# Performance work log

Hardware: AMD Instinct MI355X
Metric: run time of the kernel (lower is better)

The kernel has to match this reference:

```python
import jax, jax.numpy as jnp
import numpy as np

B, L, S, D, H = 2, 384, 384, 512, 256
BASE_TEMP = 10.0
LN_EPS = 1e-5


def setup_inputs() -> dict:
    key = jax.random.key(0)
    ks = jax.random.split(key, 12)
    return {
        "q": jax.random.normal(ks[0], (B, L, D), jnp.float32),
        "k": jax.random.normal(ks[1], (B, S, D), jnp.float32),
        "q_global": jax.random.normal(ks[2], (B, D), jnp.float32),
        "k_global": jax.random.normal(ks[3], (B, D), jnp.float32),
        "W1": jax.random.normal(ks[4], (4 * D, H), jnp.float32) * (1.0 / np.sqrt(4 * D)),
        "b1": jnp.zeros((H,), jnp.float32),
        "gamma": jnp.ones((H,), jnp.float32),
        "beta": jnp.zeros((H,), jnp.float32),
        "W2": jax.random.normal(ks[5], (H, 1), jnp.float32) * (1.0 / np.sqrt(H)),
        "b2": jnp.zeros((1,), jnp.float32),
        "gumbel_u": jax.random.uniform(ks[6], (B, L, S, 2), jnp.float32),
    }


def reference(q, k, q_global, k_global, W1, b1, gamma, beta, W2, b2, gumbel_u):
    d = q.shape[-1]
    # Decompose Linear(4D,H) on the [q, k, q_global, k_global] concat into
    # four per-tensor projections; sum broadcasts to the pairwise grid.
    Wq, Wk, Wqg, Wkg = jnp.split(W1, 4, axis=0)  # each [D,H]
    hq = q @ Wq + (q_global @ Wqg)[:, None, :]   # [B,L,H]
    hk = k @ Wk + (k_global @ Wkg)[:, None, :]   # [B,S,H]
    h = hq[:, :, None, :] + hk[:, None, :, :] + b1  # [B,L,S,H]
    h = jax.nn.gelu(h, approximate=False)
    mu = jnp.mean(h, axis=-1, keepdims=True)
    var = jnp.mean(jnp.square(h - mu), axis=-1, keepdims=True)
    h = (h - mu) * jax.lax.rsqrt(var + LN_EPS) * gamma + beta
    thresholds = (h @ W2)[..., 0] + b2[0]  # [B,L,S]
    sim = jnp.einsum("bld,bsd->bls", q, k) / jnp.sqrt(jnp.float32(d))
    logits = (sim - thresholds) / BASE_TEMP
    binary_logits = jnp.stack([-logits, logits], axis=-1)  # [B,L,S,2]
    u = jnp.clip(gumbel_u, 1e-6, 1.0 - 1e-6)
    g = -jnp.log(-jnp.log(u))
    soft = jax.nn.softmax(binary_logits + g, axis=-1)  # tau=1.0
    hard = jax.nn.one_hot(jnp.argmax(soft, axis=-1), 2, dtype=soft.dtype)
    y = hard + soft - jax.lax.stop_gradient(soft)  # straight-through
    return y[..., 1][:, None, :, :]  # [B,1,L,S]
```

## Files before the change

kernel.cpp:

```cpp
#include <hip/hip_runtime.h>
#include <hip/hip_bf16.h>
#include <math.h>

#define Bb 2
#define Lq 384
#define Sk 384
#define Dd 512
#define Hh 256

#define LIST_CAP 65536
#define NROWS (2 * Bb * Lq)

#define HQD_OFF  0
#define HKD_OFF  (HQD_OFF + Bb*Lq*Hh*8)
#define PART_OFF (HKD_OFF + Bb*Sk*Hh*8)
#define GQD_OFF  (PART_OFF + NROWS*4*Hh*8)
#define GKD_OFF  (GQD_OFF + Bb*Hh*8)
#define HQ_OFF   (GKD_OFF + Bb*Hh*8)
#define HK_OFF   (HQ_OFF + Bb*Lq*Hh*4)
#define SIM0_OFF (HK_OFF + Bb*Sk*Hh*4)
#define SIM1_OFF (SIM0_OFF + Bb*Lq*Sk*4)
#define SCAL_OFF (SIM1_OFF + Bb*Lq*Sk*4)
#define CNT_OFF  (SCAL_OFF + 64)
#define LIST_OFF (CNT_OFF + 64)

__global__ __launch_bounds__(256) void proj_fused_kernel(
    const float* __restrict__ q, const float* __restrict__ k,
    const float* __restrict__ qg, const float* __restrict__ kg,
    const float* __restrict__ W1,
    const float* __restrict__ gam, const float* __restrict__ bet,
    const float* __restrict__ W2, const float* __restrict__ b2,
    double* __restrict__ gq_d, double* __restrict__ gk_d,
    float* __restrict__ scal, int* __restrict__ cnt,
    double* __restrict__ part)
{
    __shared__ double red[64][5];
    __shared__ float2 red2[256];
    __shared__ __align__(16) float tile[4][128];
    int bx  = blockIdx.x;
    int tid = threadIdx.x;
    if (bx < 16) {
        int isK = bx & 1;
        int b   = (bx >> 1) & 1;
        int hc  = bx >> 2;
        int hl  = tid >> 2;
        int dp  = tid & 3;
        int h   = hc * 64 + hl;
        const float* gv = (isK ? kg : qg) + b * Dd;
        const float* wp = W1 + (isK ? 3 : 2) * Dd * Hh + h;
        int d0 = dp * 128;
        double a0 = 0, a1 = 0, a2 = 0, a3 = 0;
        for (int i = 0; i < 128; i += 4) {
            int d = d0 + i;
            a0 = fma((double)gv[d + 0], (double)wp[(d + 0) * Hh], a0);
            a1 = fma((double)gv[d + 1], (double)wp[(d + 1) * Hh], a1);
            a2 = fma((double)gv[d + 2], (double)wp[(d + 2) * Hh], a2);
            a3 = fma((double)gv[d + 3], (double)wp[(d + 3) * Hh], a3);
        }
        red[hl][dp] = ((a0 + a1) + (a2 + a3));
        __syncthreads();
        if (dp == 0) {
            double s = (red[hl][0] + red[hl][1]) + (red[hl][2] + red[hl][3]);
            (isK ? gk_d : gq_d)[b * Hh + h] = s;
        }
    } else if (bx == 16) {
        if (tid == 0) *cnt = 0;
        float w2v = W2[tid];
        red2[tid] = make_float2(gam[tid] * w2v, bet[tid] * w2v);
        __syncthreads();
        for (int o = 128; o > 0; o >>= 1) {
            if (tid < o) {
                red2[tid].x += red2[tid + o].x;
                red2[tid].y += red2[tid + o].y;
            }
            __syncthreads();
        }
        if (tid == 0) {
            scal[0] = red2[0].x;
            scal[1] = red2[0].y + b2[0];
        }
    } else {
        int bxp = bx - 17;
        int ds  = bxp & 3;
        int rgid = bxp >> 2;
        bool isQ = rgid < 192;
        int bb = isQ ? rgid : rgid - 192;
        int b  = bb / 96;
        int rg = bb % 96;
        const float* src = isQ ? q : k;
        int woff = isQ ? 0 : Dd * Hh;
        int rowbase = b * Lq + rg * 4;

        if (tid < 128) {
            int row = tid >> 5;
            int c4  = (tid & 31) << 2;
            *reinterpret_cast<float4*>(&tile[row][c4]) =
                *reinterpret_cast<const float4*>(
                    src + (size_t)(rowbase + row) * Dd + ds * 128 + c4);
        }
        __syncthreads();

        const float* wp = W1 + woff + (ds * 128) * Hh + tid;
        double a0 = 0.0, a1 = 0.0, a2 = 0.0, a3 = 0.0;
#pragma unroll 2
        for (int d4 = 0; d4 < 128; d4 += 4) {
            double w0 = (double)wp[(d4 + 0) * Hh];
            double w1 = (double)wp[(d4 + 1) * Hh];
            double w2 = (double)wp[(d4 + 2) * Hh];
            double w3 = (double)wp[(d4 + 3) * Hh];
            float4 t0 = *reinterpret_cast<const float4*>(&tile[0][d4]);
            float4 t1 = *reinterpret_cast<const float4*>(&tile[1][d4]);
            float4 t2 = *reinterpret_cast<const float4*>(&tile[2][d4]);
            float4 t3 = *reinterpret_cast<const float4*>(&tile[3][d4]);
            a0 = fma((double)t0.x, w0, a0); a0 = fma((double)t0.y, w1, a0);
            a0 = fma((double)t0.z, w2, a0); a0 = fma((double)t0.w, w3, a0);
            a1 = fma((double)t1.x, w0, a1); a1 = fma((double)t1.y, w1, a1);
            a1 = fma((double)t1.z, w2, a1); a1 = fma((double)t1.w, w3, a1);
            a2 = fma((double)t2.x, w0, a2); a2 = fma((double)t2.y, w1, a2);
            a2 = fma((double)t2.z, w2, a2); a2 = fma((double)t2.w, w3, a2);
            a3 = fma((double)t3.x, w0, a3); a3 = fma((double)t3.y, w1, a3);
            a3 = fma((double)t3.z, w2, a3); a3 = fma((double)t3.w, w3, a3);
        }
        int rowglob = (isQ ? 0 : Bb * Lq) + rowbase;
        size_t obase = ((size_t)rowglob * 4 + ds) * Hh + tid;
        part[obase]           = a0;
        part[obase + 4 * Hh]  = a1;
        part[obase + 8 * Hh]  = a2;
        part[obase + 12 * Hh] = a3;
    }
}

__global__ __launch_bounds__(256) void finalize_kernel(
    const double* __restrict__ part,
    const double* __restrict__ gq_d, const double* __restrict__ gk_d,
    const float* __restrict__ b1,
    double* __restrict__ hq_d, double* __restrict__ hk_d,
    float* __restrict__ hq, float* __restrict__ hk)
{
    int tid = threadIdx.x;
    int bx  = blockIdx.x;
#pragma unroll
    for (int r = 0; r < 2; ++r) {
        int rowglob = bx * 2 + r;
        bool isQ = rowglob < Bb * Lq;
        int rr = isQ ? rowglob : rowglob - Bb * Lq;
        int b  = rr / Lq;
        size_t pbase = ((size_t)rowglob * 4) * Hh + tid;
        double p0 = part[pbase];
        double p1 = part[pbase + 1 * Hh];
        double p2 = part[pbase + 2 * Hh];
        double p3 = part[pbase + 3 * Hh];
        double gl = (isQ ? gq_d : gk_d)[b * Hh + tid];
        double tot = ((p0 + p1) + (p2 + p3)) + gl;
        size_t o = (size_t)rr * Hh + tid;
        if (isQ) {
            hq_d[o] = tot;
            hq[o]   = (float)(tot + (double)b1[tid]);
        } else {
            hk_d[o] = tot;
            hk[o]   = (float)tot;
        }
    }
}

__global__ __launch_bounds__(256) void sim_kernel(
    const float* __restrict__ q, const float* __restrict__ k,
    float* __restrict__ sim01)
{
    __shared__ __align__(16) float qs[32][132];
    __shared__ __align__(16) float ks[32][132];
    int tid = threadIdx.x;
    int bx = blockIdx.x;
    int kc = (bx >= Bb * 144) ? 1 : 0;
    int r  = bx - kc * Bb * 144;
    int b  = r / 144;  r %= 144;
    int lt = r / 12, st = r % 12;
    int tl = tid >> 4, ts = tid & 15;
    const float* qb = q + (b * Lq + lt * 32) * Dd;
    const float* kb = k + (b * Sk + st * 32) * Dd;
    float a00 = 0.f, a01 = 0.f, a10 = 0.f, a11 = 0.f;
    for (int c = kc * 256; c < kc * 256 + 256; c += 128) {
        __syncthreads();
        for (int i = tid; i < 1024; i += 256) {
            int row = i >> 5;
            int c4  = (i & 31) << 2;
            *reinterpret_cast<float4*>(&qs[row][c4]) =
                *reinterpret_cast<const float4*>(qb + row * Dd + c + c4);
            *reinterpret_cast<float4*>(&ks[row][c4]) =
                *reinterpret_cast<const float4*>(kb + row * Dd + c + c4);
        }
        __syncthreads();
#pragma unroll 2
        for (int dd = 0; dd < 128; dd += 4) {
            float4 q0 = *reinterpret_cast<const float4*>(&qs[tl][dd]);
            float4 q1 = *reinterpret_cast<const float4*>(&qs[tl + 16][dd]);
            float4 k0 = *reinterpret_cast<const float4*>(&ks[ts][dd]);
            float4 k1 = *reinterpret_cast<const float4*>(&ks[ts + 16][dd]);
            a00 = fmaf(q0.x, k0.x, a00); a00 = fmaf(q0.y, k0.y, a00);
            a00 = fmaf(q0.z, k0.z, a00); a00 = fmaf(q0.w, k0.w, a00);
            a01 = fmaf(q0.x, k1.x, a01); a01 = fmaf(q0.y, k1.y, a01);
            a01 = fmaf(q0.z, k1.z, a01); a01 = fmaf(q0.w, k1.w, a01);
            a10 = fmaf(q1.x, k0.x, a10); a10 = fmaf(q1.y, k0.y, a10);
            a10 = fmaf(q1.z, k0.z, a10); a10 = fmaf(q1.w, k0.w, a10);
            a11 = fmaf(q1.x, k1.x, a11); a11 = fmaf(q1.y, k1.y, a11);
            a11 = fmaf(q1.z, k1.z, a11); a11 = fmaf(q1.w, k1.w, a11);
        }
    }
    const float sc = 0.04419417382415922f;
    float* dst = sim01 + kc * (Bb * Lq * Sk);
    int l0 = lt * 32 + tl, s0 = st * 32 + ts;
    dst[(b * Lq + l0)      * Sk + s0]      = a00 * sc;
    dst[(b * Lq + l0)      * Sk + s0 + 16] = a01 * sc;
    dst[(b * Lq + l0 + 16) * Sk + s0]      = a10 * sc;
    dst[(b * Lq + l0 + 16) * Sk + s0 + 16] = a11 * sc;
}

__device__ __forceinline__ void gelu2t(float2 hqv, float2 hkv, float2 gwv,
                                       float2& s1, float2& s2, float2& sw)
{
    const float K1 = -2.30220815f;
    const float K2 = -0.10294325f;
    float xa = hqv.x + hkv.x,  xb = hqv.y + hkv.y;
    float x2a = xa * xa,       x2b = xb * xb;
    float pa = fmaf(K2, x2a, K1), pb = fmaf(K2, x2b, K1);
    float za = xa * pa,        zb = xb * pb;
    float ea = __builtin_amdgcn_exp2f(za);
    float eb = __builtin_amdgcn_exp2f(zb);
    float ra = __builtin_amdgcn_rcpf(1.0f + ea);
    float rb = __builtin_amdgcn_rcpf(1.0f + eb);
    float ya = (xa + xa) * ra, yb = (xb + xb) * rb;
    s1.x += ya;                s1.y += yb;
    s2.x = fmaf(ya, ya, s2.x); s2.y = fmaf(yb, yb, s2.y);
    sw.x = fmaf(ya, gwv.x, sw.x); sw.y = fmaf(yb, gwv.y, sw.y);
}

__global__ __launch_bounds__(512) void main_kernel(
    const float* __restrict__ hq, const float* __restrict__ hk,
    const float* __restrict__ sim0, const float* __restrict__ sim1,
    const float* __restrict__ gam, const float* __restrict__ W2,
    const float* __restrict__ scal,
    const float* __restrict__ gu, float* __restrict__ out,
    int* __restrict__ cnt, int* __restrict__ list)
{
    __shared__ __align__(16) float hq_t[32][260];
    __shared__ __align__(16) float hk_t[16][260];
    __shared__ __align__(16) float gw_s[256];
    int tid = threadIdx.x;
    int bx = blockIdx.x;
    int b  = bx / (12 * 24);
    int r  = bx % (12 * 24);
    int lt = r / 24, st = r % 24;

    const float* hqb = hq + (b * Lq + lt * 32) * Hh;
    const float* hkb = hk + (b * Sk + st * 16) * Hh;
#pragma unroll
    for (int i = 0; i < 4; ++i) {
        int idx4 = i * 512 + tid;
        int row  = idx4 >> 6;
        int col4 = (idx4 & 63) << 2;
        *reinterpret_cast<float4*>(&hq_t[row][col4]) =
            *reinterpret_cast<const float4*>(hqb + row * Hh + col4);
    }
#pragma unroll
    for (int i = 0; i < 2; ++i) {
        int idx4 = i * 512 + tid;
        int row  = idx4 >> 6;
        int col4 = (idx4 & 63) << 2;
        *reinterpret_cast<float4*>(&hk_t[row][col4]) =
            *reinterpret_cast<const float4*>(hkb + row * Hh + col4);
    }
    if (tid < 256) gw_s[tid] = gam[tid] * W2[tid];
    __syncthreads();
    float gwsum  = scal[0];
    float bconst = scal[1];

    int opair = tid >> 1;
    int hh    = tid & 1;
    int tl = opair >> 4, ts = opair & 15;

    float2 s1a = make_float2(0.f, 0.f), s2a = s1a, swa = s1a;
    float2 s1b = s1a, s2b = s1a, swb = s1a;
    int h0 = hh << 7;
#pragma unroll 2
    for (int h4 = h0; h4 < h0 + 128; h4 += 4) {
        float4 ha = *reinterpret_cast<const float4*>(&hq_t[tl][h4]);
        float4 hb = *reinterpret_cast<const float4*>(&hq_t[tl + 16][h4]);
        float4 kk = *reinterpret_cast<const float4*>(&hk_t[ts][h4]);
        float4 g4 = *reinterpret_cast<const float4*>(&gw_s[h4]);
        gelu2t(make_float2(ha.x, ha.y), make_float2(kk.x, kk.y),
               make_float2(g4.x, g4.y), s1a, s2a, swa);
        gelu2t(make_float2(ha.z, ha.w), make_float2(kk.z, kk.w),
               make_float2(g4.z, g4.w), s1a, s2a, swa);
        gelu2t(make_float2(hb.x, hb.y), make_float2(kk.x, kk.y),
               make_float2(g4.x, g4.y), s1b, s2b, swb);
        gelu2t(make_float2(hb.z, hb.w), make_float2(kk.z, kk.w),
               make_float2(g4.z, g4.w), s1b, s2b, swb);
    }
    float S1a = s1a.x + s1a.y;  S1a += __shfl_xor(S1a, 1, 64);
    float S2a = s2a.x + s2a.y;  S2a += __shfl_xor(S2a, 1, 64);
    float SWa = swa.x + swa.y;  SWa += __shfl_xor(SWa, 1, 64);
    float S1b = s1b.x + s1b.y;  S1b += __shfl_xor(S1b, 1, 64);
    float S2b = s2b.x + s2b.y;  S2b += __shfl_xor(S2b, 1, 64);
    float SWb = swb.x + swb.y;  SWb += __shfl_xor(SWb, 1, 64);

    float S1 = hh ? S1b : S1a;
    float S2 = hh ? S2b : S2a;
    float SW = 0.5f * (hh ? SWb : SWa);
    float mu   = S1 * (1.0f / 512.0f);
    float var  = S2 * (1.0f / 1024.0f) - mu * mu;
    float rstd = rsqrtf(var + 1e-5f);
    float thr  = rstd * (SW - mu * gwsum) + bconst;

    int l = lt * 32 + tl + hh * 16, s = st * 16 + ts;
    int idx = (b * Lq + l) * Sk + s;
    float  sv = sim0[idx] + sim1[idx];
    float2 uv = reinterpret_cast<const float2*>(gu)[idx];
    float u0 = fminf(fmaxf(uv.x, 1e-6f), 1.0f - 1e-6f);
    float u1 = fminf(fmaxf(uv.y, 1e-6f), 1.0f - 1e-6f);
    float g0 = -logf(-logf(u0));
    float g1 = -logf(-logf(u1));
    float t  = 0.2f * (sv - thr) + (g1 - g0);
    out[idx] = t > 0.0f ? 1.0f : 0.0f;
    if (fabsf(t) < 2e-3f) {
        int p = atomicAdd(cnt, 1);
        if (p < LIST_CAP) list[p] = idx;
    }
}

__global__ __launch_bounds__(256) void cleanup_kernel(
    const float* __restrict__ q, const float* __restrict__ k,
    const double* __restrict__ hq_d, const double* __restrict__ hk_d,
    const float* __restrict__ b1,
    const float* __restrict__ gam, const float* __restrict__ bet,
    const float* __restrict__ W2, const float* __restrict__ b2,
    const float* __restrict__ gu, float* __restrict__ out,
    const int* __restrict__ cnt, const int* __restrict__ list)
{
    __shared__ double s0[256], s1[256], s2[256], s3[256];
    int tid = threadIdx.x;
    int n = *cnt;
    if (n > LIST_CAP) n = LIST_CAP;
    if (n == 0) return;

    double gw  = (double)gam[tid] * (double)W2[tid];
    double b1d = (double)b1[tid];
    s0[tid] = (double)bet[tid] * (double)W2[tid];
    s1[tid] = gw;
    __syncthreads();
    for (int o = 128; o > 0; o >>= 1) {
        if (tid < o) { s0[tid] += s0[tid + o]; s1[tid] += s1[tid + o]; }
        __syncthreads();
    }
    double bconst = s0[0] + (double)b2[0];
    double gwsum  = s1[0];
    __syncthreads();

    for (int it = blockIdx.x; it < n; it += gridDim.x) {
        int idx = list[it];
        int b   = idx / (Lq * Sk);
        int rem = idx % (Lq * Sk);
        int l = rem / Sk, s = rem % Sk;
        double x = (hq_d[(b * Lq + l) * Hh + tid]
                  + hk_d[(b * Sk + s) * Hh + tid]) + b1d;
        double y = 0.5 * x * (1.0 + erf(x * 0.70710678118654752440));
        const float* qrow = q + (b * Lq + l) * Dd;
        const float* krow = k + (b * Sk + s) * Dd;
        double sp = (double)qrow[tid] * (double)krow[tid]
                  + (double)qrow[tid + 256] * (double)krow[tid + 256];
        s0[tid] = y; s1[tid] = y * y; s2[tid] = y * gw; s3[tid] = sp;
        __syncthreads();
        for (int o = 128; o > 0; o >>= 1) {
            if (tid < o) {
                s0[tid] += s0[tid + o]; s1[tid] += s1[tid + o];
                s2[tid] += s2[tid + o]; s3[tid] += s3[tid + o];
            }
            __syncthreads();
        }
        if (tid == 0) {
            double mu   = s0[0] * (1.0 / 256.0);
            double var  = s1[0] * (1.0 / 256.0) - mu * mu;
            double rstd = 1.0 / sqrt(var + 1e-5);
            double thr  = rstd * (s2[0] - mu * gwsum) + bconst;
            double simv = s3[0] / 22.627416997969522;
            float2 uv = reinterpret_cast<const float2*>(gu)[idx];
            double u0 = fmin(fmax((double)uv.x, 1e-6), 1.0 - 1e-6);
            double u1 = fmin(fmax((double)uv.y, 1e-6), 1.0 - 1e-6);
            double g0 = -log(-log(u0));
            double g1 = -log(-log(u1));
            double t  = 0.2 * (simv - thr) + (g1 - g0);
            out[idx] = t > 0.0 ? 1.0f : 0.0f;
        }
        __syncthreads();
    }
}

extern "C" void kernel_launch(void* const* d_in, const int* in_sizes, int n_in,
                              void* d_out, int out_size, void* d_ws, size_t ws_size,
                              hipStream_t stream)
{
    const float* q   = (const float*)d_in[0];
    const float* k   = (const float*)d_in[1];
    const float* qg  = (const float*)d_in[2];
    const float* kg  = (const float*)d_in[3];
    const float* W1  = (const float*)d_in[4];
    const float* b1  = (const float*)d_in[5];
    const float* gam = (const float*)d_in[6];
    const float* bet = (const float*)d_in[7];
    const float* W2  = (const float*)d_in[8];
    const float* b2  = (const float*)d_in[9];
    const float* gu  = (const float*)d_in[10];
    float* out = (float*)d_out;

    char*   ws   = (char*)d_ws;
    double* hq_d = (double*)(ws + HQD_OFF);
    double* hk_d = (double*)(ws + HKD_OFF);
    double* part = (double*)(ws + PART_OFF);
    double* gq_d = (double*)(ws + GQD_OFF);
    double* gk_d = (double*)(ws + GKD_OFF);
    float*  hq   = (float*)(ws + HQ_OFF);
    float*  hk   = (float*)(ws + HK_OFF);
    float*  sim0 = (float*)(ws + SIM0_OFF);
    float*  sim1 = (float*)(ws + SIM1_OFF);
    float*  scal = (float*)(ws + SCAL_OFF);
    int*    cnt  = (int*)(ws + CNT_OFF);
    int*    list = (int*)(ws + LIST_OFF);

    proj_fused_kernel<<<17 + NROWS, 256, 0, stream>>>(
        q, k, qg, kg, W1, gam, bet, W2, b2, gq_d, gk_d, scal, cnt, part);
    finalize_kernel<<<NROWS / 2, 256, 0, stream>>>(
        part, gq_d, gk_d, b1, hq_d, hk_d, hq, hk);
    sim_kernel<<<2 * Bb * 144, 256, 0, stream>>>(q, k, sim0);
    main_kernel<<<Bb * 12 * 24, 512, 0, stream>>>(
        hq, hk, sim0, sim1, gam, W2, scal, gu, out, cnt, list);
    cleanup_kernel<<<768, 256, 0, stream>>>(
        q, k, hq_d, hk_d, b1, gam, bet, W2, b2, gu, out, cnt, list);
}
```

Measured before the change: 157.2 us.

## Retile sim GEMM to 64x64 register-blocked tiles with 8-way split-K partial planes

The q·k similarity kernel moves from 32x32 tiles with 2x2 outputs per thread and a 2-way K split to 64x64 tiles with 4x4 register-blocked outputs per thread and an 8-way K split. Operands are stored transposed in shared memory, so each thread issues one float4 load per operand per k-step. The aim is more FMA work per shared-memory load. In exchange, the main kernel must read and sum 8 partial planes instead of 2, which adds global traffic to that kernel, and the transposed scalar shared-memory stores may cause bank conflicts.

```diff
diff --git a/kernel.cpp b/kernel.cpp
--- a/kernel.cpp
+++ b/kernel.cpp
@@ -10,6 +10,7 @@
 
 #define LIST_CAP 65536
 #define NROWS (2 * Bb * Lq)
+#define PLANE (Bb * Lq * Sk)
 
 #define HQD_OFF  0
 #define HKD_OFF  (HQD_OFF + Bb*Lq*Hh*8)
@@ -18,9 +19,8 @@
 #define GKD_OFF  (GQD_OFF + Bb*Hh*8)
 #define HQ_OFF   (GKD_OFF + Bb*Hh*8)
 #define HK_OFF   (HQ_OFF + Bb*Lq*Hh*4)
-#define SIM0_OFF (HK_OFF + Bb*Sk*Hh*4)
-#define SIM1_OFF (SIM0_OFF + Bb*Lq*Sk*4)
-#define SCAL_OFF (SIM1_OFF + Bb*Lq*Sk*4)
+#define SIM_OFF  (HK_OFF + Bb*Sk*Hh*4)
+#define SCAL_OFF (SIM_OFF + 8*PLANE*4)
 #define CNT_OFF  (SCAL_OFF + 64)
 #define LIST_OFF (CNT_OFF + 64)
 
@@ -165,54 +165,71 @@
 
 __global__ __launch_bounds__(256) void sim_kernel(
     const float* __restrict__ q, const float* __restrict__ k,
-    float* __restrict__ sim01)
-{
-    __shared__ __align__(16) float qs[32][132];
-    __shared__ __align__(16) float ks[32][132];
+    float* __restrict__ simP)
+{
+    __shared__ __align__(16) float qs_t[64][68];
+    __shared__ __align__(16) float ks_t[64][68];
     int tid = threadIdx.x;
-    int bx = blockIdx.x;
-    int kc = (bx >= Bb * 144) ? 1 : 0;
-    int r  = bx - kc * Bb * 144;
-    int b  = r / 144;  r %= 144;
-    int lt = r / 12, st = r % 12;
+    int bx  = blockIdx.x;
+    int kc  = bx / 72;
+    int r   = bx % 72;
+    int b   = r / 36;  r %= 36;
+    int lt  = r / 6,  st = r % 6;
+
+    const float* qb = q + (size_t)(b * Lq + lt * 64) * Dd + kc * 64;
+    const float* kb = k + (size_t)(b * Sk + st * 64) * Dd + kc * 64;
+#pragma unroll
+    for (int it = 0; it < 4; ++it) {
+        int i   = it * 256 + tid;
+        int row = i >> 4;
+        int c4  = (i & 15) << 2;
+        float4 vq = *reinterpret_cast<const float4*>(qb + (size_t)row * Dd + c4);
+        float4 vk = *reinterpret_cast<const float4*>(kb + (size_t)row * Dd + c4);
+        qs_t[c4 + 0][row] = vq.x; qs_t[c4 + 1][row] = vq.y;
+        qs_t[c4 + 2][row] = vq.z; qs_t[c4 + 3][row] = vq.w;
+        ks_t[c4 + 0][row] = vk.x; ks_t[c4 + 1][row] = vk.y;
+        ks_t[c4 + 2][row] = vk.z; ks_t[c4 + 3][row] = vk.w;
+    }
+    __syncthreads();
+
     int tl = tid >> 4, ts = tid & 15;
-    const float* qb = q + (b * Lq + lt * 32) * Dd;
-    const float* kb = k + (b * Sk + st * 32) * Dd;
-    float a00 = 0.f, a01 = 0.f, a10 = 0.f, a11 = 0.f;
-    for (int c = kc * 256; c < kc * 256 + 256; c += 128) {
-        __syncthreads();
-        for (int i = tid; i < 1024; i += 256) {
-            int row = i >> 5;
-            int c4  = (i & 31) << 2;
-            *reinterpret_cast<float4*>(&qs[row][c4]) =
-                *reinterpret_cast<const float4*>(qb + row * Dd + c + c4);
-            *reinterpret_cast<float4*>(&ks[row][c4]) =
-                *reinterpret_cast<const float4*>(kb + row * Dd + c + c4);
-        }
-        __syncthreads();
-#pragma unroll 2
-        for (int dd = 0; dd < 128; dd += 4) {
-            float4 q0 = *reinterpret_cast<const float4*>(&qs[tl][dd]);
-            float4 q1 = *reinterpret_cast<const float4*>(&qs[tl + 16][dd]);
-            float4 k0 = *reinterpret_cast<const float4*>(&ks[ts][dd]);
-            float4 k1 = *reinterpret_cast<const float4*>(&ks[ts + 16][dd]);
-            a00 = fmaf(q0.x, k0.x, a00); a00 = fmaf(q0.y, k0.y, a00);
-            a00 = fmaf(q0.z, k0.z, a00); a00 = fmaf(q0.w, k0.w, a00);
-            a01 = fmaf(q0.x, k1.x, a01); a01 = fmaf(q0.y, k1.y, a01);
-            a01 = fmaf(q0.z, k1.z, a01); a01 = fmaf(q0.w, k1.w, a01);
-            a10 = fmaf(q1.x, k0.x, a10); a10 = fmaf(q1.y, k0.y, a10);
-            a10 = fmaf(q1.z, k0.z, a10); a10 = fmaf(q1.w, k0.w, a10);
-            a11 = fmaf(q1.x, k1.x, a11); a11 = fmaf(q1.y, k1.y, a11);
-            a11 = fmaf(q1.z, k1.z, a11); a11 = fmaf(q1.w, k1.w, a11);
-        }
-    }
+    float acc[4][4];
+#pragma unroll
+    for (int i = 0; i < 4; ++i)
+#pragma unroll
+        for (int j = 0; j < 4; ++j) acc[i][j] = 0.f;
+
+#pragma unroll 4
+    for (int dd = 0; dd < 64; ++dd) {
+        float4 qa = *reinterpret_cast<const float4*>(&qs_t[dd][4 * tl]);
+        float4 kb4 = *reinterpret_cast<const float4*>(&ks_t[dd][4 * ts]);
+        acc[0][0] = fmaf(qa.x, kb4.x, acc[0][0]);
+        acc[0][1] = fmaf(qa.x, kb4.y, acc[0][1]);
+        acc[0][2] = fmaf(qa.x, kb4.z, acc[0][2]);
+        acc[0][3] = fmaf(qa.x, kb4.w, acc[0][3]);
+        acc[1][0] = fmaf(qa.y, kb4.x, acc[1][0]);
+        acc[1][1] = fmaf(qa.y, kb4.y, acc[1][1]);
+        acc[1][2] = fmaf(qa.y, kb4.z, acc[1][2]);
+        acc[1][3] = fmaf(qa.y, kb4.w, acc[1][3]);
+        acc[2][0] = fmaf(qa.z, kb4.x, acc[2][0]);
+        acc[2][1] = fmaf(qa.z, kb4.y, acc[2][1]);
+        acc[2][2] = fmaf(qa.z, kb4.z, acc[2][2]);
+        acc[2][3] = fmaf(qa.z, kb4.w, acc[2][3]);
+        acc[3][0] = fmaf(qa.w, kb4.x, acc[3][0]);
+        acc[3][1] = fmaf(qa.w, kb4.y, acc[3][1]);
+        acc[3][2] = fmaf(qa.w, kb4.z, acc[3][2]);
+        acc[3][3] = fmaf(qa.w, kb4.w, acc[3][3]);
+    }
+
     const float sc = 0.04419417382415922f;
-    float* dst = sim01 + kc * (Bb * Lq * Sk);
-    int l0 = lt * 32 + tl, s0 = st * 32 + ts;
-    dst[(b * Lq + l0)      * Sk + s0]      = a00 * sc;
-    dst[(b * Lq + l0)      * Sk + s0 + 16] = a01 * sc;
-    dst[(b * Lq + l0 + 16) * Sk + s0]      = a10 * sc;
-    dst[(b * Lq + l0 + 16) * Sk + s0 + 16] = a11 * sc;
+    float* dst = simP + (size_t)kc * PLANE;
+    int l0 = lt * 64 + 4 * tl, s0 = st * 64 + 4 * ts;
+#pragma unroll
+    for (int i = 0; i < 4; ++i) {
+        float4 v = make_float4(acc[i][0] * sc, acc[i][1] * sc,
+                               acc[i][2] * sc, acc[i][3] * sc);
+        *reinterpret_cast<float4*>(&dst[(size_t)(b * Lq + l0 + i) * Sk + s0]) = v;
+    }
 }
 
 __device__ __forceinline__ void gelu2t(float2 hqv, float2 hkv, float2 gwv,
@@ -236,7 +253,7 @@
 
 __global__ __launch_bounds__(512) void main_kernel(
     const float* __restrict__ hq, const float* __restrict__ hk,
-    const float* __restrict__ sim0, const float* __restrict__ sim1,
+    const float* __restrict__ simP,
     const float* __restrict__ gam, const float* __restrict__ W2,
     const float* __restrict__ scal,
     const float* __restrict__ gu, float* __restrict__ out,
@@ -313,7 +330,9 @@
 
     int l = lt * 32 + tl + hh * 16, s = st * 16 + ts;
     int idx = (b * Lq + l) * Sk + s;
-    float  sv = sim0[idx] + sim1[idx];
+    float sv = 0.f;
+#pragma unroll
+    for (int p = 0; p < 8; ++p) sv += simP[(size_t)p * PLANE + idx];
     float2 uv = reinterpret_cast<const float2*>(gu)[idx];
     float u0 = fminf(fmaxf(uv.x, 1e-6f), 1.0f - 1e-6f);
     float u1 = fminf(fmaxf(uv.y, 1e-6f), 1.0f - 1e-6f);
@@ -419,8 +438,7 @@
     double* gk_d = (double*)(ws + GKD_OFF);
     float*  hq   = (float*)(ws + HQ_OFF);
     float*  hk   = (float*)(ws + HK_OFF);
-    float*  sim0 = (float*)(ws + SIM0_OFF);
-    float*  sim1 = (float*)(ws + SIM1_OFF);
+    float*  simP = (float*)(ws + SIM_OFF);
     float*  scal = (float*)(ws + SCAL_OFF);
     int*    cnt  = (int*)(ws + CNT_OFF);
     int*    list = (int*)(ws + LIST_OFF);
@@ -429,9 +447,9 @@
         q, k, qg, kg, W1, gam, bet, W2, b2, gq_d, gk_d, scal, cnt, part);
     finalize_kernel<<<NROWS / 2, 256, 0, stream>>>(
         part, gq_d, gk_d, b1, hq_d, hk_d, hq, hk);
-    sim_kernel<<<2 * Bb * 144, 256, 0, stream>>>(q, k, sim0);
+    sim_kernel<<<576, 256, 0, stream>>>(q, k, simP);
     main_kernel<<<Bb * 12 * 24, 512, 0, stream>>>(
-        hq, hk, sim0, sim1, gam, W2, scal, gu, out, cnt, list);
+        hq, hk, simP, gam, W2, scal, gu, out, cnt, list);
     cleanup_kernel<<<768, 256, 0, stream>>>(
         q, k, hq_d, hk_d, b1, gam, bet, W2, b2, gu, out, cnt, list);
 }
```

Measured after the change: 157.2 us. No clear change (-0.0%).

## Fuse q·k similarity computation into main kernel, drop separate sim kernel

Applied to the files above, without the earlier changes.

Removes the standalone sim_kernel and its two split-K partial buffers, and computes the scaled q·k dot product inside main_kernel using the same 32x16 tile. Each thread pair splits D into halves per 128-column chunk and combines them with a lane shuffle. Shared memory is reused between the q/k staging tiles and the hq/hk tiles. This saves a kernel launch and the round trip of sim values through global memory. In exchange main_kernel takes on extra serial work, and k rows are reloaded more often because the tiles are smaller than sim_kernel's 32x32.

```diff
diff --git a/kernel.cpp b/kernel.cpp
--- a/kernel.cpp
+++ b/kernel.cpp
@@ -18,9 +18,7 @@
 #define GKD_OFF  (GQD_OFF + Bb*Hh*8)
 #define HQ_OFF   (GKD_OFF + Bb*Hh*8)
 #define HK_OFF   (HQ_OFF + Bb*Lq*Hh*4)
-#define SIM0_OFF (HK_OFF + Bb*Sk*Hh*4)
-#define SIM1_OFF (SIM0_OFF + Bb*Lq*Sk*4)
-#define SCAL_OFF (SIM1_OFF + Bb*Lq*Sk*4)
+#define SCAL_OFF (HK_OFF + Bb*Sk*Hh*4)
 #define CNT_OFF  (SCAL_OFF + 64)
 #define LIST_OFF (CNT_OFF + 64)
 
@@ -163,58 +161,6 @@
     }
 }
 
-__global__ __launch_bounds__(256) void sim_kernel(
-    const float* __restrict__ q, const float* __restrict__ k,
-    float* __restrict__ sim01)
-{
-    __shared__ __align__(16) float qs[32][132];
-    __shared__ __align__(16) float ks[32][132];
-    int tid = threadIdx.x;
-    int bx = blockIdx.x;
-    int kc = (bx >= Bb * 144) ? 1 : 0;
-    int r  = bx - kc * Bb * 144;
-    int b  = r / 144;  r %= 144;
-    int lt = r / 12, st = r % 12;
-    int tl = tid >> 4, ts = tid & 15;
-    const float* qb = q + (b * Lq + lt * 32) * Dd;
-    const float* kb = k + (b * Sk + st * 32) * Dd;
-    float a00 = 0.f, a01 = 0.f, a10 = 0.f, a11 = 0.f;
-    for (int c = kc * 256; c < kc * 256 + 256; c += 128) {
-        __syncthreads();
-        for (int i = tid; i < 1024; i += 256) {
-            int row = i >> 5;
-            int c4  = (i & 31) << 2;
-            *reinterpret_cast<float4*>(&qs[row][c4]) =
-                *reinterpret_cast<const float4*>(qb + row * Dd + c + c4);
-            *reinterpret_cast<float4*>(&ks[row][c4]) =
-                *reinterpret_cast<const float4*>(kb + row * Dd + c + c4);
-        }
-        __syncthreads();
-#pragma unroll 2
-        for (int dd = 0; dd < 128; dd += 4) {
-            float4 q0 = *reinterpret_cast<const float4*>(&qs[tl][dd]);
-            float4 q1 = *reinterpret_cast<const float4*>(&qs[tl + 16][dd]);
-            float4 k0 = *reinterpret_cast<const float4*>(&ks[ts][dd]);
-            float4 k1 = *reinterpret_cast<const float4*>(&ks[ts + 16][dd]);
-            a00 = fmaf(q0.x, k0.x, a00); a00 = fmaf(q0.y, k0.y, a00);
-            a00 = fmaf(q0.z, k0.z, a00); a00 = fmaf(q0.w, k0.w, a00);
-            a01 = fmaf(q0.x, k1.x, a01); a01 = fmaf(q0.y, k1.y, a01);
-            a01 = fmaf(q0.z, k1.z, a01); a01 = fmaf(q0.w, k1.w, a01);
-            a10 = fmaf(q1.x, k0.x, a10); a10 = fmaf(q1.y, k0.y, a10);
-            a10 = fmaf(q1.z, k0.z, a10); a10 = fmaf(q1.w, k0.w, a10);
-            a11 = fmaf(q1.x, k1.x, a11); a11 = fmaf(q1.y, k1.y, a11);
-            a11 = fmaf(q1.z, k1.z, a11); a11 = fmaf(q1.w, k1.w, a11);
-        }
-    }
-    const float sc = 0.04419417382415922f;
-    float* dst = sim01 + kc * (Bb * Lq * Sk);
-    int l0 = lt * 32 + tl, s0 = st * 32 + ts;
-    dst[(b * Lq + l0)      * Sk + s0]      = a00 * sc;
-    dst[(b * Lq + l0)      * Sk + s0 + 16] = a01 * sc;
-    dst[(b * Lq + l0 + 16) * Sk + s0]      = a10 * sc;
-    dst[(b * Lq + l0 + 16) * Sk + s0 + 16] = a11 * sc;
-}
-
 __device__ __forceinline__ void gelu2t(float2 hqv, float2 hkv, float2 gwv,
                                        float2& s1, float2& s2, float2& sw)
 {
@@ -235,22 +181,66 @@
 }
 
 __global__ __launch_bounds__(512) void main_kernel(
+    const float* __restrict__ q, const float* __restrict__ k,
     const float* __restrict__ hq, const float* __restrict__ hk,
-    const float* __restrict__ sim0, const float* __restrict__ sim1,
     const float* __restrict__ gam, const float* __restrict__ W2,
     const float* __restrict__ scal,
     const float* __restrict__ gu, float* __restrict__ out,
     int* __restrict__ cnt, int* __restrict__ list)
 {
-    __shared__ __align__(16) float hq_t[32][260];
-    __shared__ __align__(16) float hk_t[16][260];
-    __shared__ __align__(16) float gw_s[256];
+    __shared__ __align__(16) float smem[32 * 260 + 16 * 260 + 256];
+    float (*qs)[132]   = (float (*)[132])smem;
+    float (*ks)[132]   = (float (*)[132])(smem + 32 * 132);
+    float (*hq_t)[260] = (float (*)[260])smem;
+    float (*hk_t)[260] = (float (*)[260])(smem + 32 * 260);
+    float* gw_s        = smem + 32 * 260 + 16 * 260;
+
     int tid = threadIdx.x;
     int bx = blockIdx.x;
     int b  = bx / (12 * 24);
     int r  = bx % (12 * 24);
     int lt = r / 24, st = r % 24;
 
+    int opair = tid >> 1;
+    int hh    = tid & 1;
+    int tl = opair >> 4, ts = opair & 15;
+
+    const float* qb = q + (size_t)(b * Lq + lt * 32) * Dd;
+    const float* kb = k + (size_t)(b * Sk + st * 16) * Dd;
+    float sva = 0.f, svb = 0.f;
+    for (int c = 0; c < Dd; c += 128) {
+        __syncthreads();
+        for (int i = tid; i < 1536; i += 512) {
+            if (i < 1024) {
+                int row = i >> 5, c4 = (i & 31) << 2;
+                *reinterpret_cast<float4*>(&qs[row][c4]) =
+                    *reinterpret_cast<const float4*>(qb + (size_t)row * Dd + c + c4);
+            } else {
+                int j = i - 1024;
+                int row = j >> 5, c4 = (j & 31) << 2;
+                *reinterpret_cast<float4*>(&ks[row][c4]) =
+                    *reinterpret_cast<const float4*>(kb + (size_t)row * Dd + c + c4);
+            }
+        }
+        __syncthreads();
+        int d0 = hh << 6;
+#pragma unroll 4
+        for (int d4 = d0; d4 < d0 + 64; d4 += 4) {
+            float4 qa = *reinterpret_cast<const float4*>(&qs[tl][d4]);
+            float4 qc = *reinterpret_cast<const float4*>(&qs[tl + 16][d4]);
+            float4 kk = *reinterpret_cast<const float4*>(&ks[ts][d4]);
+            sva = fmaf(qa.x, kk.x, sva); sva = fmaf(qa.y, kk.y, sva);
+            sva = fmaf(qa.z, kk.z, sva); sva = fmaf(qa.w, kk.w, sva);
+            svb = fmaf(qc.x, kk.x, svb); svb = fmaf(qc.y, kk.y, svb);
+            svb = fmaf(qc.z, kk.z, svb); svb = fmaf(qc.w, kk.w, svb);
+        }
+    }
+    sva += __shfl_xor(sva, 1, 64);
+    svb += __shfl_xor(svb, 1, 64);
+    const float sc = 0.04419417382415922f;
+    sva *= sc; svb *= sc;
+
+    __syncthreads();
     const float* hqb = hq + (b * Lq + lt * 32) * Hh;
     const float* hkb = hk + (b * Sk + st * 16) * Hh;
 #pragma unroll
@@ -273,10 +263,6 @@
     __syncthreads();
     float gwsum  = scal[0];
     float bconst = scal[1];
-
-    int opair = tid >> 1;
-    int hh    = tid & 1;
-    int tl = opair >> 4, ts = opair & 15;
 
     float2 s1a = make_float2(0.f, 0.f), s2a = s1a, swa = s1a;
     float2 s1b = s1a, s2b = s1a, swb = s1a;
@@ -306,6 +292,7 @@
     float S1 = hh ? S1b : S1a;
     float S2 = hh ? S2b : S2a;
     float SW = 0.5f * (hh ? SWb : SWa);
+    float sv = hh ? svb : sva;
     float mu   = S1 * (1.0f / 512.0f);
     float var  = S2 * (1.0f / 1024.0f) - mu * mu;
     float rstd = rsqrtf(var + 1e-5f);
@@ -313,7 +300,6 @@
 
     int l = lt * 32 + tl + hh * 16, s = st * 16 + ts;
     int idx = (b * Lq + l) * Sk + s;
-    float  sv = sim0[idx] + sim1[idx];
     float2 uv = reinterpret_cast<const float2*>(gu)[idx];
     float u0 = fminf(fmaxf(uv.x, 1e-6f), 1.0f - 1e-6f);
     float u1 = fminf(fmaxf(uv.y, 1e-6f), 1.0f - 1e-6f);
@@ -419,8 +405,6 @@
     double* gk_d = (double*)(ws + GKD_OFF);
     float*  hq   = (float*)(ws + HQ_OFF);
     float*  hk   = (float*)(ws + HK_OFF);
-    float*  sim0 = (float*)(ws + SIM0_OFF);
-    float*  sim1 = (float*)(ws + SIM1_OFF);
     float*  scal = (float*)(ws + SCAL_OFF);
     int*    cnt  = (int*)(ws + CNT_OFF);
     int*    list = (int*)(ws + LIST_OFF);
@@ -429,9 +413,8 @@
         q, k, qg, kg, W1, gam, bet, W2, b2, gq_d, gk_d, scal, cnt, part);
     finalize_kernel<<<NROWS / 2, 256, 0, stream>>>(
         part, gq_d, gk_d, b1, hq_d, hk_d, hq, hk);
-    sim_kernel<<<2 * Bb * 144, 256, 0, stream>>>(q, k, sim0);
     main_kernel<<<Bb * 12 * 24, 512, 0, stream>>>(
-        hq, hk, sim0, sim1, gam, W2, scal, gu, out, cnt, list);
+        q, k, hq, hk, gam, W2, scal, gu, out, cnt, list);
     cleanup_kernel<<<768, 256, 0, stream>>>(
         q, k, hq_d, hk_d, b1, gam, bet, W2, b2, gu, out, cnt, list);
 }
```

Result: slower. 161.5 us (+2.7%).
